# Kernel optimization log

Hardware: AMD Instinct MI355X
Metric: run time of the kernel (lower is better)

## Reference

```python
import jax, jax.numpy as jnp
import numpy as np

B, C, H, W = 8, 128, 64, 64


def conv1x1(x, w, b):
    # x: [B,C,H,W], w: [Cout,Cin], b: [Cout] -> [B,Cout,H,W]
    return jnp.einsum('bchw,oc->bohw', x, w) + b[None, :, None, None]


def setup_inputs() -> dict:
    key = jax.random.key(0)
    ks = jax.random.split(key, 8)
    scale = 1.0 / np.sqrt(C)  # keep QK logits in a sane range
    return {
        'cur': jax.random.normal(ks[0], (B, C, H, W), jnp.float32),
        'ref': jax.random.normal(ks[1], (B, C, H, W), jnp.float32),
        'theta_w': jax.random.normal(ks[2], (C, C), jnp.float32) * scale,
        'theta_b': jnp.zeros((C,), jnp.float32),
        'phi_w': jax.random.normal(ks[3], (C, C), jnp.float32) * scale,
        'phi_b': jnp.zeros((C,), jnp.float32),
        'W_w': jax.random.normal(ks[4], (C, C), jnp.float32) * scale,
        'W_b': jnp.zeros((C,), jnp.float32),
    }


def reference(cur, ref, theta_w, theta_b, phi_w, phi_b, W_w, W_b):
    b, c, h, w = cur.shape
    n = h * w
    # x = theta(ref): [B, N, C]  (queries come from the reference frame)
    x = conv1x1(ref, theta_w, theta_b).reshape(b, c, n).transpose(0, 2, 1)
    # y = phi(cur): [B, C, N]
    y = conv1x1(cur, phi_w, phi_b).reshape(b, c, n)
    # attn: [B, N_ref, N_cur], softmax over the NON-standard axis 1 (ref positions)
    attn = jax.nn.softmax(jnp.einsum('bnc,bcm->bnm', x, y), axis=1)
    # z = attn @ x: [B, N, C] -> [B, C, H, W]
    z = jnp.einsum('bnm,bmc->bnc', attn, x).transpose(0, 2, 1).reshape(b, c, h, w)
    return conv1x1(z, W_w, W_b)
```

## Files before the change

### kernel.cpp

```cpp
#include <hip/hip_runtime.h>
#include <hip/hip_bf16.h>

#define BB 8
#define CC 128
#define NN 4096
#define LOG2E 1.44269504088896340736f

typedef __attribute__((ext_vector_type(8))) short bf16x8;
typedef __attribute__((ext_vector_type(16))) float f32x16;

static __device__ __forceinline__ unsigned short f2bfu(float f) {
  unsigned int x = __float_as_uint(f);
  x += 0x7fffu + ((x >> 16) & 1u);
  return (unsigned short)(x >> 16);
}
static __device__ __forceinline__ unsigned int packbf(float a, float b) {
  return (unsigned int)f2bfu(a) | ((unsigned int)f2bfu(b) << 16);
}
static __device__ __forceinline__ float bfu2f(unsigned short u) {
  return __uint_as_float((unsigned int)u << 16);
}
static __device__ __forceinline__ float fexp2(float x) {
  return __builtin_amdgcn_exp2f(x);
}
static __device__ __forceinline__ f32x16 zero16() {
  f32x16 z;
#pragma unroll
  for (int i = 0; i < 16; ++i) z[i] = 0.f;
  return z;
}
union Frag { int i[4]; unsigned int u[4]; bf16x8 v; };

static __device__ __forceinline__ unsigned int cvtpk(float a, float b) {
  unsigned int r;
  asm("v_cvt_pk_bf16_f32 %0, %1, %2" : "=v"(r) : "v"(a), "v"(b));
  return r;
}
static __device__ __forceinline__ void pl32swap(unsigned int& d, unsigned int& s) {
  asm volatile("v_permlane32_swap_b32 %0, %1" : "+v"(d), "+v"(s));
}

#define GLD16(gp, lp)                                                     \
  __builtin_amdgcn_global_load_lds(                                       \
      (const __attribute__((address_space(1))) unsigned int*)(gp),        \
      (__attribute__((address_space(3))) unsigned int*)(lp), 16, 0, 0)

#define ROWPAT(rg, q2) (((rg) & 3) + 8 * ((rg) >> 2) + 4 * (q2))

static __device__ __forceinline__ void make_pa(const f32x16& s, Frag& lo, Frag& hi) {
  float p[16];
#pragma unroll
  for (int rg = 0; rg < 16; ++rg) p[rg] = fexp2(s[rg]);
  unsigned int a0 = cvtpk(p[0], p[1]),   b0 = cvtpk(p[4], p[5]);
  pl32swap(a0, b0);
  unsigned int a1 = cvtpk(p[2], p[3]),   b1 = cvtpk(p[6], p[7]);
  pl32swap(a1, b1);
  lo.u[0] = a0; lo.u[1] = a1; lo.u[2] = b0; lo.u[3] = b1;
  unsigned int c0 = cvtpk(p[8], p[9]),   d0 = cvtpk(p[12], p[13]);
  pl32swap(c0, d0);
  unsigned int c1 = cvtpk(p[10], p[11]), d1 = cvtpk(p[14], p[15]);
  pl32swap(c1, d1);
  hi.u[0] = c0; hi.u[1] = c1; hi.u[2] = d0; hi.u[3] = d1;
}

__global__ __launch_bounds__(256, 4) void nl_conv2m(
    const float* __restrict__ ref, const float* __restrict__ theta_w,
    const float* __restrict__ theta_b,
    const float* __restrict__ cur, const float* __restrict__ phi_w,
    const float* __restrict__ phi_b,
    unsigned short* __restrict__ Xnc, unsigned short* __restrict__ Xcn,
    unsigned short* __restrict__ Ync)
{
  __shared__ float sm[64 * 129];
  const int z  = blockIdx.z;
  const float* in   = z ? cur : ref;
  const float* w    = z ? phi_w : theta_w;
  const float* bias = z ? phi_b : theta_b;
  unsigned short* out_nc = z ? Ync : Xnc;
  unsigned short* out_cn = z ? nullptr : Xcn;
  const float nc_scale = z ? 1.0f : LOG2E;

  const int b  = blockIdx.y;
  const int n0 = blockIdx.x * 64;
  const int t  = threadIdx.x;
  const int wave = t >> 6, lane = t & 63, q2 = lane >> 5, cm = lane & 31;

#pragma unroll
  for (int k = 0; k < 16; ++k) {
    int flat = t + 256 * k;
    int c = flat >> 5, jp = flat & 31;
    float2 v = *(const float2*)&in[(size_t)b * CC * NN + (size_t)c * NN + n0 + jp * 2];
    sm[c * 64 + jp * 2]     = v.x;
    sm[c * 64 + jp * 2 + 1] = v.y;
  }

  bf16x8 wf[8];
  const int o0 = wave * 32 + cm;
#pragma unroll
  for (int k = 0; k < 8; ++k) {
    const float* wp = &w[o0 * CC + k * 16 + q2 * 8];
    float4 w0 = *(const float4*)wp, w1 = *(const float4*)(wp + 4);
    Frag f;
    f.u[0] = packbf(w0.x, w0.y); f.u[1] = packbf(w0.z, w0.w);
    f.u[2] = packbf(w1.x, w1.y); f.u[3] = packbf(w1.z, w1.w);
    wf[k] = f.v;
  }
  __syncthreads();

  f32x16 acc[2];
  acc[0] = zero16(); acc[1] = zero16();
#pragma unroll
  for (int k = 0; k < 8; ++k) {
#pragma unroll
    for (int jt = 0; jt < 2; ++jt) {
      int base = (k * 16 + q2 * 8) * 64 + jt * 32 + cm;
      Frag xb;
      xb.u[0] = cvtpk(sm[base],       sm[base + 64]);
      xb.u[1] = cvtpk(sm[base + 128], sm[base + 192]);
      xb.u[2] = cvtpk(sm[base + 256], sm[base + 320]);
      xb.u[3] = cvtpk(sm[base + 384], sm[base + 448]);
      acc[jt] = __builtin_amdgcn_mfma_f32_32x32x16_bf16(wf[k], xb.v, acc[jt], 0, 0, 0);
    }
  }
  __syncthreads();

#pragma unroll
  for (int jt = 0; jt < 2; ++jt)
#pragma unroll
    for (int rg = 0; rg < 16; ++rg) {
      int o = wave * 32 + ROWPAT(rg, q2);
      sm[(jt * 32 + cm) * 129 + o] = acc[jt][rg] + bias[o];
    }
  __syncthreads();

#pragma unroll
  for (int k = 0; k < 16; ++k) {
    int flat = t + 256 * k;
    int cp = flat & 63, jj = flat >> 6;
    float f0 = sm[jj * 129 + cp * 2] * nc_scale;
    float f1 = sm[jj * 129 + cp * 2 + 1] * nc_scale;
    *(unsigned int*)(out_nc + ((size_t)b * NN + n0 + jj) * CC + cp * 2) = packbf(f0, f1);
  }
  if (out_cn) {
#pragma unroll
    for (int k = 0; k < 16; ++k) {
      int flat = t + 256 * k;
      int jp = flat & 31, c = flat >> 5;
      float f0 = sm[(jp * 2) * 129 + c], f1 = sm[(jp * 2 + 1) * 129 + c];
      *(unsigned int*)(out_cn + ((size_t)b * CC + c) * NN + n0 + jp * 2) = packbf(f0, f1);
    }
  }
}

__global__ __launch_bounds__(256, 4) void nl_stats4(
    const unsigned short* __restrict__ Xnc, const unsigned short* __restrict__ Ync,
    float* __restrict__ Lpart)
{
  __shared__ unsigned short Xt[2][64 * 128];
  __shared__ float sL[2][2][2][32];
  const int b = blockIdx.z, nq = blockIdx.y, mstrip = blockIdx.x;
  const int t = threadIdx.x;
  const int wave = t >> 6, lane = t & 63, q2 = lane >> 5, cm = lane & 31;
  const int mq = wave & 1, nh = wave >> 1;
  const int m0w = mstrip * 128 + mq * 64;

  bf16x8 bf[2][8];
#pragma unroll
  for (int ct = 0; ct < 2; ++ct)
#pragma unroll
    for (int k = 0; k < 8; ++k)
      bf[ct][k] = *(const bf16x8*)(Ync + ((size_t)b * NN + m0w + ct * 32 + cm) * CC + k * 16 + q2 * 8);

  {
    const int n0 = nq * 1024;
#pragma unroll
    for (int i = 0; i < 4; ++i) {
      int slot = i * 256 + t;
      int row = slot >> 4, g = (slot & 15) ^ (row & 7);
      GLD16(Xnc + ((size_t)b * NN + n0 + row) * CC + g * 8, &Xt[0][0] + i * 2048 + wave * 512);
    }
  }

  float runL[2] = {0.f, 0.f};
#pragma unroll 2
  for (int nt = 0; nt < 16; ++nt) {
    __syncthreads();
    if (nt < 15) {
      const int n0 = nq * 1024 + (nt + 1) * 64;
      unsigned short* dst = &Xt[(nt + 1) & 1][0];
#pragma unroll
      for (int i = 0; i < 4; ++i) {
        int slot = i * 256 + t;
        int row = slot >> 4, g = (slot & 15) ^ (row & 7);
        GLD16(Xnc + ((size_t)b * NN + n0 + row) * CC + g * 8, dst + i * 2048 + wave * 512);
      }
    }
    const unsigned short* src = &Xt[nt & 1][0];
    f32x16 acc0 = zero16(), acc1 = zero16();
#pragma unroll
    for (int k = 0; k < 8; ++k) {
      bf16x8 av = *(const bf16x8*)&src[(nh * 32 + cm) * 128 + (((k << 1) | q2) ^ (cm & 7)) * 8];
      acc0 = __builtin_amdgcn_mfma_f32_32x32x16_bf16(av, bf[0][k], acc0, 0, 0, 0);
      acc1 = __builtin_amdgcn_mfma_f32_32x32x16_bf16(av, bf[1][k], acc1, 0, 0, 0);
    }
#pragma unroll
    for (int rg = 0; rg < 16; ++rg) {
      runL[0] += fexp2(acc0[rg]);
      runL[1] += fexp2(acc1[rg]);
    }
  }
#pragma unroll
  for (int ct = 0; ct < 2; ++ct) runL[ct] += __shfl_xor(runL[ct], 32);
  if (q2 == 0) {
    sL[nh][mq][0][cm] = runL[0];
    sL[nh][mq][1][cm] = runL[1];
  }
  __syncthreads();
  if (t < 128) {
    int mq2 = t >> 6, ct2 = (t >> 5) & 1, cm2 = t & 31;
    float L = sL[0][mq2][ct2][cm2] + sL[1][mq2][ct2][cm2];
    Lpart[((size_t)nq * BB + b) * NN + mstrip * 128 + mq2 * 64 + ct2 * 32 + cm2] = L;
  }
}

__global__ __launch_bounds__(256) void nl_scalev(
    const float* __restrict__ Lp, unsigned short* __restrict__ Xcn)
{
  __shared__ float iL[64];
  const int b = blockIdx.y, mc = blockIdx.x;
  const int t = threadIdx.x;
  const int m0 = mc * 64;
  if (t < 64) {
    size_t idx = (size_t)b * NN + m0 + t;
    float L = Lp[idx] + Lp[(size_t)BB * NN + idx] + Lp[(size_t)2 * BB * NN + idx] +
              Lp[(size_t)3 * BB * NN + idx];
    iL[t] = 1.0f / L;
  }
  __syncthreads();
#pragma unroll
  for (int r = 0; r < 4; ++r) {
    int idx = r * 256 + t;
    int c = idx >> 3, mg = idx & 7;
    size_t base = ((size_t)b * CC + c) * NN + m0 + mg * 8;
    Frag x; x.v = *(const bf16x8*)(Xcn + base);
    const float* il = &iL[mg * 8];
    Frag o;
    o.u[0] = packbf(bfu2f(x.u[0] & 0xffff) * il[0], bfu2f(x.u[0] >> 16) * il[1]);
    o.u[1] = packbf(bfu2f(x.u[1] & 0xffff) * il[2], bfu2f(x.u[1] >> 16) * il[3]);
    o.u[2] = packbf(bfu2f(x.u[2] & 0xffff) * il[4], bfu2f(x.u[2] >> 16) * il[5]);
    o.u[3] = packbf(bfu2f(x.u[3] & 0xffff) * il[6], bfu2f(x.u[3] >> 16) * il[7]);
    *(bf16x8*)(Xcn + base) = o.v;
  }
}

__global__ __launch_bounds__(256, 2) void nl_pass2e2(
    const unsigned short* __restrict__ Xnc, const unsigned short* __restrict__ Ync,
    const unsigned short* __restrict__ Xsc,
    unsigned short* __restrict__ Zpart)
{
  __shared__ unsigned short Yt[2][64 * 128];
  __shared__ unsigned short Xv[2][128 * 64];
  const int b = blockIdx.z, mhalf = blockIdx.y, nstrip = blockIdx.x;
  const int t = threadIdx.x;
  const int wave = t >> 6, lane = t & 63, q2 = lane >> 5, cm = lane & 31;

  bf16x8 af[8];
#pragma unroll
  for (int k = 0; k < 8; ++k)
    af[k] = *(const bf16x8*)(Xnc +
        ((size_t)b * NN + nstrip * 128 + wave * 32 + cm) * CC + k * 16 + q2 * 8);

  f32x16 z[4];
#pragma unroll
  for (int ct = 0; ct < 4; ++ct) z[ct] = zero16();

  {
    const int m0g = mhalf * 2048;
#pragma unroll
    for (int i = 0; i < 4; ++i) {
      int slot = i * 256 + t;
      int row = slot >> 4, g = (slot & 15) ^ (row & 7);
      GLD16(Ync + ((size_t)b * NN + m0g + row) * CC + g * 8, &Yt[0][0] + i * 2048 + wave * 512);
    }
#pragma unroll
    for (int i = 0; i < 4; ++i) {
      int slot = i * 256 + t;
      int row = slot >> 3, g = (slot & 7) ^ (row & 7);
      GLD16(Xsc + ((size_t)b * CC + row) * NN + m0g + g * 8, &Xv[0][0] + i * 2048 + wave * 512);
    }
  }

#define P2_ITER(BUF, MT)                                                       \
  do {                                                                         \
    __syncthreads();                                                           \
    if ((MT) < 31) {                                                           \
      const int m0g = mhalf * 2048 + ((MT) + 1) * 64;                          \
      unsigned short* Yd = &Yt[(BUF) ^ 1][0];                                  \
      unsigned short* Xd = &Xv[(BUF) ^ 1][0];                                  \
      _Pragma("unroll")                                                        \
      for (int i = 0; i < 4; ++i) {                                            \
        int slot = i * 256 + t;                                                \
        int row = slot >> 4, g = (slot & 15) ^ (row & 7);                      \
        GLD16(Ync + ((size_t)b * NN + m0g + row) * CC + g * 8,                 \
              Yd + i * 2048 + wave * 512);                                     \
      }                                                                        \
      _Pragma("unroll")                                                        \
      for (int i = 0; i < 4; ++i) {                                            \
        int slot = i * 256 + t;                                                \
        int row = slot >> 3, g = (slot & 7) ^ (row & 7);                       \
        GLD16(Xsc + ((size_t)b * CC + row) * NN + m0g + g * 8,                 \
              Xd + i * 2048 + wave * 512);                                     \
      }                                                                        \
    }                                                                          \
    const unsigned short* Ys = &Yt[BUF][0];                                    \
    f32x16 s0 = zero16(), s1 = zero16();                                       \
    __builtin_amdgcn_s_setprio(1);                                             \
    _Pragma("unroll")                                                          \
    for (int k = 0; k < 8; ++k) {                                              \
      const int ch = (((k << 1) | q2) ^ (cm & 7)) * 8;                         \
      bf16x8 av0 = *(const bf16x8*)&Ys[cm * 128 + ch];                         \
      bf16x8 av1 = *(const bf16x8*)&Ys[(32 + cm) * 128 + ch];                  \
      s0 = __builtin_amdgcn_mfma_f32_32x32x16_bf16(av0, af[k], s0, 0, 0, 0);   \
      s1 = __builtin_amdgcn_mfma_f32_32x32x16_bf16(av1, af[k], s1, 0, 0, 0);   \
    }                                                                          \
    __builtin_amdgcn_s_setprio(0);                                             \
    Frag pa[4];                                                                \
    make_pa(s0, pa[0], pa[1]);                                                 \
    make_pa(s1, pa[2], pa[3]);                                                 \
    const unsigned short* Xs = &Xv[BUF][0];                                    \
    __builtin_amdgcn_s_setprio(1);                                             \
    _Pragma("unroll")                                                          \
    for (int ks = 0; ks < 4; ++ks) {                                           \
      const int ch = (((ks << 1) | q2) ^ (cm & 7)) * 8;                        \
      _Pragma("unroll")                                                        \
      for (int ct = 0; ct < 4; ++ct) {                                         \
        bf16x8 xv = *(const bf16x8*)&Xs[(ct * 32 + cm) * 64 + ch];             \
        z[ct] = __builtin_amdgcn_mfma_f32_32x32x16_bf16(pa[ks].v, xv, z[ct], 0, 0, 0); \
      }                                                                        \
    }                                                                          \
    __builtin_amdgcn_s_setprio(0);                                             \
  } while (0)

  for (int mt2 = 0; mt2 < 16; ++mt2) {
    P2_ITER(0, mt2 * 2);
    P2_ITER(1, mt2 * 2 + 1);
  }
#undef P2_ITER

  unsigned short* Zp = Zpart + ((size_t)mhalf * BB + b) * NN * CC;
#pragma unroll
  for (int ct = 0; ct < 4; ++ct)
#pragma unroll
    for (int rg = 0; rg < 16; ++rg) {
      int n = nstrip * 128 + wave * 32 + ROWPAT(rg, q2);
      Zp[(size_t)n * CC + ct * 32 + cm] = f2bfu(z[ct][rg]);
    }
}

__global__ __launch_bounds__(256) void nl_convw2(
    const unsigned short* __restrict__ Zpart, const float* __restrict__ w,
    const float* __restrict__ bias, float* __restrict__ out)
{
  __shared__ unsigned short Zt[64 * 128];
  const int b = blockIdx.y, nstrip = blockIdx.x;
  const int t = threadIdx.x;
  const int wave = t >> 6, lane = t & 63, q2 = lane >> 5, cm = lane & 31;
  const int oh = wave & 1, nh2 = wave >> 1;

  const unsigned short* Z0 = Zpart + ((size_t)b * NN + nstrip * 64) * CC;
  const unsigned short* Z1 = Z0 + (size_t)BB * NN * CC;
#pragma unroll
  for (int i = 0; i < 4; ++i) {
    int slot = i * 256 + t;
    int row = slot >> 4, g = slot & 15;
    size_t off = (size_t)row * CC + g * 8;
    Frag a, c2, o;
    a.v  = *(const bf16x8*)(Z0 + off);
    c2.v = *(const bf16x8*)(Z1 + off);
#pragma unroll
    for (int w2 = 0; w2 < 4; ++w2) {
      float lo = bfu2f((unsigned short)(a.u[w2] & 0xffff)) +
                 bfu2f((unsigned short)(c2.u[w2] & 0xffff));
      float hi = bfu2f((unsigned short)(a.u[w2] >> 16)) +
                 bfu2f((unsigned short)(c2.u[w2] >> 16));
      o.u[w2] = packbf(lo, hi);
    }
    *(bf16x8*)&Zt[row * 128 + ((g ^ (row & 7)) * 8)] = o.v;
  }

  bf16x8 wf[2][8];
#pragma unroll
  for (int s2 = 0; s2 < 2; ++s2)
#pragma unroll
    for (int k = 0; k < 8; ++k) {
      const float* wp = &w[(oh * 64 + s2 * 32 + cm) * CC + k * 16 + q2 * 8];
      float4 w0 = *(const float4*)wp, w1 = *(const float4*)(wp + 4);
      Frag f;
      f.u[0] = packbf(w0.x, w0.y); f.u[1] = packbf(w0.z, w0.w);
      f.u[2] = packbf(w1.x, w1.y); f.u[3] = packbf(w1.z, w1.w);
      wf[s2][k] = f.v;
    }
  __syncthreads();

  f32x16 z[2];
  z[0] = zero16(); z[1] = zero16();
#pragma unroll
  for (int k = 0; k < 8; ++k) {
    bf16x8 bv = *(const bf16x8*)&Zt[(nh2 * 32 + cm) * 128 + (((k << 1) | q2) ^ (cm & 7)) * 8];
#pragma unroll
    for (int i = 0; i < 2; ++i)
      z[i] = __builtin_amdgcn_mfma_f32_32x32x16_bf16(wf[i][k], bv, z[i], 0, 0, 0);
  }

#pragma unroll
  for (int i = 0; i < 2; ++i)
#pragma unroll
    for (int rg = 0; rg < 16; ++rg) {
      int o = oh * 64 + i * 32 + ROWPAT(rg, q2);
      int n = nstrip * 64 + nh2 * 32 + cm;
      out[(size_t)b * CC * NN + (size_t)o * NN + n] = z[i][rg] + bias[o];
    }
}

extern "C" void kernel_launch(void* const* d_in, const int* in_sizes, int n_in,
                              void* d_out, int out_size, void* d_ws, size_t ws_size,
                              hipStream_t stream) {
  const float* cur     = (const float*)d_in[0];
  const float* ref     = (const float*)d_in[1];
  const float* theta_w = (const float*)d_in[2];
  const float* theta_b = (const float*)d_in[3];
  const float* phi_w   = (const float*)d_in[4];
  const float* phi_b   = (const float*)d_in[5];
  const float* Ww      = (const float*)d_in[6];
  const float* Wb      = (const float*)d_in[7];
  float* out = (float*)d_out;

  unsigned short* Xnc = (unsigned short*)d_ws;
  unsigned short* Ync = Xnc + (size_t)BB * NN * CC;
  unsigned short* Xcn = Ync + (size_t)BB * NN * CC;
  float* Lpart = (float*)(Xcn + (size_t)BB * NN * CC);
  unsigned short* Zpart = (unsigned short*)(Lpart + (size_t)4 * BB * NN);

  dim3 blk(256);
  nl_conv2m  <<<dim3(64, BB, 2), blk, 0, stream>>>(ref, theta_w, theta_b,
                                                   cur, phi_w, phi_b, Xnc, Xcn, Ync);
  nl_stats4  <<<dim3(32, 4, BB), blk, 0, stream>>>(Xnc, Ync, Lpart);
  nl_scalev  <<<dim3(64, BB), blk, 0, stream>>>(Lpart, Xcn);
  nl_pass2e2 <<<dim3(32, 2, BB), blk, 0, stream>>>(Xnc, Ync, Xcn, Zpart);
  nl_convw2  <<<dim3(64, BB), blk, 0, stream>>>(Zpart, Ww, Wb, out);
}
```

Before: 231.4 us.

## Split pass2 waves into n-pairs by m-halves with LDS partial-sum reduction

Pass 2 now gives each pair of waves 64 query rows, with each wave covering half of the 64-wide m tile. This halves the LDS reads of Y per wave and reuses each X-value fragment for two MFMAs instead of one. The two waves' partial z accumulators are combined through LDS at the end. The LDS swizzle for 128-wide rows is widened from xor 7 to xor 15 in the stats and pass2 kernels to cut bank conflicts. The cost is doubled accumulator registers (8 f32x16 per wave) and an extra reduction step at the end.

Result: slower. 335.2 us (+44.9%).

```diff
diff --git a/kernel.cpp b/kernel.cpp
--- a/kernel.cpp
+++ b/kernel.cpp
@@ -176,7 +176,7 @@
 #pragma unroll
     for (int i = 0; i < 4; ++i) {
       int slot = i * 256 + t;
-      int row = slot >> 4, g = (slot & 15) ^ (row & 7);
+      int row = slot >> 4, g = (slot & 15) ^ (row & 15);
       GLD16(Xnc + ((size_t)b * NN + n0 + row) * CC + g * 8, &Xt[0][0] + i * 2048 + wave * 512);
     }
   }
@@ -191,7 +191,7 @@
 #pragma unroll
       for (int i = 0; i < 4; ++i) {
         int slot = i * 256 + t;
-        int row = slot >> 4, g = (slot & 15) ^ (row & 7);
+        int row = slot >> 4, g = (slot & 15) ^ (row & 15);
         GLD16(Xnc + ((size_t)b * NN + n0 + row) * CC + g * 8, dst + i * 2048 + wave * 512);
       }
     }
@@ -199,7 +199,7 @@
     f32x16 acc0 = zero16(), acc1 = zero16();
 #pragma unroll
     for (int k = 0; k < 8; ++k) {
-      bf16x8 av = *(const bf16x8*)&src[(nh * 32 + cm) * 128 + (((k << 1) | q2) ^ (cm & 7)) * 8];
+      bf16x8 av = *(const bf16x8*)&src[(nh * 32 + cm) * 128 + (((k << 1) | q2) ^ (cm & 15)) * 8];
       acc0 = __builtin_amdgcn_mfma_f32_32x32x16_bf16(av, bf[0][k], acc0, 0, 0, 0);
       acc1 = __builtin_amdgcn_mfma_f32_32x32x16_bf16(av, bf[1][k], acc1, 0, 0, 0);
     }
@@ -253,108 +253,120 @@
   }
 }
 
-__global__ __launch_bounds__(256, 2) void nl_pass2e2(
+__global__ __launch_bounds__(256, 2) void nl_pass2f2(
     const unsigned short* __restrict__ Xnc, const unsigned short* __restrict__ Ync,
     const unsigned short* __restrict__ Xsc,
     unsigned short* __restrict__ Zpart)
 {
-  __shared__ unsigned short Yt[2][64 * 128];
-  __shared__ unsigned short Xv[2][128 * 64];
+  __shared__ unsigned short SB[2][16384];
   const int b = blockIdx.z, mhalf = blockIdx.y, nstrip = blockIdx.x;
   const int t = threadIdx.x;
   const int wave = t >> 6, lane = t & 63, q2 = lane >> 5, cm = lane & 31;
-
-  bf16x8 af[8];
-#pragma unroll
-  for (int k = 0; k < 8; ++k)
-    af[k] = *(const bf16x8*)(Xnc +
-        ((size_t)b * NN + nstrip * 128 + wave * 32 + cm) * CC + k * 16 + q2 * 8);
-
-  f32x16 z[4];
-#pragma unroll
-  for (int ct = 0; ct < 4; ++ct) z[ct] = zero16();
-
-  {
-    const int m0g = mhalf * 2048;
-#pragma unroll
-    for (int i = 0; i < 4; ++i) {
-      int slot = i * 256 + t;
-      int row = slot >> 4, g = (slot & 15) ^ (row & 7);
-      GLD16(Ync + ((size_t)b * NN + m0g + row) * CC + g * 8, &Yt[0][0] + i * 2048 + wave * 512);
-    }
-#pragma unroll
-    for (int i = 0; i < 4; ++i) {
-      int slot = i * 256 + t;
-      int row = slot >> 3, g = (slot & 7) ^ (row & 7);
-      GLD16(Xsc + ((size_t)b * CC + row) * NN + m0g + g * 8, &Xv[0][0] + i * 2048 + wave * 512);
-    }
-  }
-
-#define P2_ITER(BUF, MT)                                                       \
+  const int npair = wave >> 1, msub = wave & 1;
+
+  bf16x8 af[2][8];
+#pragma unroll
+  for (int g = 0; g < 2; ++g)
+#pragma unroll
+    for (int k = 0; k < 8; ++k)
+      af[g][k] = *(const bf16x8*)(Xnc +
+          ((size_t)b * NN + nstrip * 128 + npair * 64 + g * 32 + cm) * CC + k * 16 + q2 * 8);
+
+  f32x16 z[2][4];
+#pragma unroll
+  for (int g = 0; g < 2; ++g)
+#pragma unroll
+    for (int ct = 0; ct < 4; ++ct) z[g][ct] = zero16();
+
+#define STAGEF(DSTBUF, M0G)                                                    \
+  do {                                                                         \
+    unsigned short* Yd = &SB[DSTBUF][0];                                       \
+    unsigned short* Xd = &SB[DSTBUF][8192];                                    \
+    _Pragma("unroll")                                                          \
+    for (int i = 0; i < 4; ++i) {                                              \
+      int slot = i * 256 + t;                                                  \
+      int row = slot >> 4, g = (slot & 15) ^ (row & 15);                       \
+      GLD16(Ync + ((size_t)b * NN + (M0G) + row) * CC + g * 8,                 \
+            Yd + i * 2048 + wave * 512);                                       \
+    }                                                                          \
+    _Pragma("unroll")                                                          \
+    for (int i = 0; i < 4; ++i) {                                              \
+      int slot = i * 256 + t;                                                  \
+      int row = slot >> 3, g = (slot & 7) ^ (row & 7);                         \
+      GLD16(Xsc + ((size_t)b * CC + row) * NN + (M0G) + g * 8,                 \
+            Xd + i * 2048 + wave * 512);                                       \
+    }                                                                          \
+  } while (0)
+
+  STAGEF(0, mhalf * 2048);
+
+#define PF_ITER(BUF, MT)                                                       \
   do {                                                                         \
     __syncthreads();                                                           \
-    if ((MT) < 31) {                                                           \
-      const int m0g = mhalf * 2048 + ((MT) + 1) * 64;                          \
-      unsigned short* Yd = &Yt[(BUF) ^ 1][0];                                  \
-      unsigned short* Xd = &Xv[(BUF) ^ 1][0];                                  \
-      _Pragma("unroll")                                                        \
-      for (int i = 0; i < 4; ++i) {                                            \
-        int slot = i * 256 + t;                                                \
-        int row = slot >> 4, g = (slot & 15) ^ (row & 7);                      \
-        GLD16(Ync + ((size_t)b * NN + m0g + row) * CC + g * 8,                 \
-              Yd + i * 2048 + wave * 512);                                     \
-      }                                                                        \
-      _Pragma("unroll")                                                        \
-      for (int i = 0; i < 4; ++i) {                                            \
-        int slot = i * 256 + t;                                                \
-        int row = slot >> 3, g = (slot & 7) ^ (row & 7);                       \
-        GLD16(Xsc + ((size_t)b * CC + row) * NN + m0g + g * 8,                 \
-              Xd + i * 2048 + wave * 512);                                     \
-      }                                                                        \
-    }                                                                          \
-    const unsigned short* Ys = &Yt[BUF][0];                                    \
+    if ((MT) < 31) STAGEF((BUF) ^ 1, mhalf * 2048 + ((MT) + 1) * 64);          \
+    const unsigned short* Ys = &SB[BUF][0];                                    \
     f32x16 s0 = zero16(), s1 = zero16();                                       \
     __builtin_amdgcn_s_setprio(1);                                             \
     _Pragma("unroll")                                                          \
     for (int k = 0; k < 8; ++k) {                                              \
-      const int ch = (((k << 1) | q2) ^ (cm & 7)) * 8;                         \
-      bf16x8 av0 = *(const bf16x8*)&Ys[cm * 128 + ch];                         \
-      bf16x8 av1 = *(const bf16x8*)&Ys[(32 + cm) * 128 + ch];                  \
-      s0 = __builtin_amdgcn_mfma_f32_32x32x16_bf16(av0, af[k], s0, 0, 0, 0);   \
-      s1 = __builtin_amdgcn_mfma_f32_32x32x16_bf16(av1, af[k], s1, 0, 0, 0);   \
+      const int ch = (((k << 1) | q2) ^ (cm & 15)) * 8;                        \
+      bf16x8 av = *(const bf16x8*)&Ys[(msub * 32 + cm) * 128 + ch];            \
+      s0 = __builtin_amdgcn_mfma_f32_32x32x16_bf16(av, af[0][k], s0, 0, 0, 0); \
+      s1 = __builtin_amdgcn_mfma_f32_32x32x16_bf16(av, af[1][k], s1, 0, 0, 0); \
     }                                                                          \
     __builtin_amdgcn_s_setprio(0);                                             \
-    Frag pa[4];                                                                \
-    make_pa(s0, pa[0], pa[1]);                                                 \
-    make_pa(s1, pa[2], pa[3]);                                                 \
-    const unsigned short* Xs = &Xv[BUF][0];                                    \
+    Frag pa[2][2];                                                             \
+    make_pa(s0, pa[0][0], pa[0][1]);                                           \
+    make_pa(s1, pa[1][0], pa[1][1]);                                           \
+    const unsigned short* Xs = &SB[BUF][8192];                                 \
     __builtin_amdgcn_s_setprio(1);                                             \
     _Pragma("unroll")                                                          \
-    for (int ks = 0; ks < 4; ++ks) {                                           \
-      const int ch = (((ks << 1) | q2) ^ (cm & 7)) * 8;                        \
+    for (int ksl = 0; ksl < 2; ++ksl) {                                        \
+      const int ksg = msub * 2 + ksl;                                          \
+      const int ch = (((ksg << 1) | q2) ^ (cm & 7)) * 8;                       \
       _Pragma("unroll")                                                        \
       for (int ct = 0; ct < 4; ++ct) {                                         \
         bf16x8 xv = *(const bf16x8*)&Xs[(ct * 32 + cm) * 64 + ch];             \
-        z[ct] = __builtin_amdgcn_mfma_f32_32x32x16_bf16(pa[ks].v, xv, z[ct], 0, 0, 0); \
+        z[0][ct] = __builtin_amdgcn_mfma_f32_32x32x16_bf16(pa[0][ksl].v, xv, z[0][ct], 0, 0, 0); \
+        z[1][ct] = __builtin_amdgcn_mfma_f32_32x32x16_bf16(pa[1][ksl].v, xv, z[1][ct], 0, 0, 0); \
       }                                                                        \
     }                                                                          \
     __builtin_amdgcn_s_setprio(0);                                             \
   } while (0)
 
   for (int mt2 = 0; mt2 < 16; ++mt2) {
-    P2_ITER(0, mt2 * 2);
-    P2_ITER(1, mt2 * 2 + 1);
-  }
-#undef P2_ITER
-
-  unsigned short* Zp = Zpart + ((size_t)mhalf * BB + b) * NN * CC;
-#pragma unroll
-  for (int ct = 0; ct < 4; ++ct)
-#pragma unroll
-    for (int rg = 0; rg < 16; ++rg) {
-      int n = nstrip * 128 + wave * 32 + ROWPAT(rg, q2);
-      Zp[(size_t)n * CC + ct * 32 + cm] = f2bfu(z[ct][rg]);
-    }
+    PF_ITER(0, mt2 * 2);
+    PF_ITER(1, mt2 * 2 + 1);
+  }
+#undef PF_ITER
+#undef STAGEF
+
+  __syncthreads();
+  float* zl = (float*)&SB[0][0] + npair * 8192;
+  if (msub == 1) {
+#pragma unroll
+    for (int g = 0; g < 2; ++g)
+#pragma unroll
+      for (int ct = 0; ct < 4; ++ct)
+#pragma unroll
+        for (int rg = 0; rg < 16; ++rg)
+          zl[(g * 32 + ROWPAT(rg, q2)) * 128 + ct * 32 + cm] = z[g][ct][rg];
+  }
+  __syncthreads();
+  if (msub == 0) {
+    unsigned short* Zp = Zpart + ((size_t)mhalf * BB + b) * NN * CC;
+#pragma unroll
+    for (int g = 0; g < 2; ++g)
+#pragma unroll
+      for (int ct = 0; ct < 4; ++ct)
+#pragma unroll
+        for (int rg = 0; rg < 16; ++rg) {
+          int nl = g * 32 + ROWPAT(rg, q2);
+          int n = nstrip * 128 + npair * 64 + nl;
+          Zp[(size_t)n * CC + ct * 32 + cm] =
+              f2bfu(z[g][ct][rg] + zl[nl * 128 + ct * 32 + cm]);
+        }
+  }
 }
 
 __global__ __launch_bounds__(256) void nl_convw2(
@@ -446,6 +458,6 @@
                                                    cur, phi_w, phi_b, Xnc, Xcn, Ync);
   nl_stats4  <<<dim3(32, 4, BB), blk, 0, stream>>>(Xnc, Ync, Lpart);
   nl_scalev  <<<dim3(64, BB), blk, 0, stream>>>(Lpart, Xcn);
-  nl_pass2e2 <<<dim3(32, 2, BB), blk, 0, stream>>>(Xnc, Ync, Xcn, Zpart);
+  nl_pass2f2 <<<dim3(32, 2, BB), blk, 0, stream>>>(Xnc, Ync, Xcn, Zpart);
   nl_convw2  <<<dim3(64, BB), blk, 0, stream>>>(Zpart, Ww, Wb, out);
 }
```
